# Kernel optimization log

Measured on AMD Instinct MI355X. Metric: run time of the kernel, lower is better.

The kernel has to match this reference:

```python
import jax, jax.numpy as jnp
import numpy as np

N, D_IN, D_OUT = 8192, 1024, 1024

def setup_inputs() -> dict:
    key = jax.random.key(0)
    kx, kq, kk, kv = jax.random.split(key, 4)
    s = 1.0 / np.sqrt(D_IN)
    return {
        "x": jax.random.normal(kx, (N, D_IN), dtype=jnp.float32),
        "Wq": jax.random.uniform(kq, (D_OUT, D_IN), dtype=jnp.float32, minval=-s, maxval=s),
        "Wk": jax.random.uniform(kk, (D_OUT, D_IN), dtype=jnp.float32, minval=-s, maxval=s),
        "Wv": jax.random.uniform(kv, (D_OUT, D_IN), dtype=jnp.float32, minval=-s, maxval=s),
    }

def reference(x, Wq, Wk, Wv):
    # Linear layers: y = x @ W.T (no bias, qkv_bias=False)
    q = x @ Wq.T  # [N, d_out]
    k = x @ Wk.T
    v = x @ Wv.T
    scores = q @ k.T  # [N, N]
    weights = jax.nn.softmax(scores / jnp.sqrt(jnp.float32(k.shape[-1])), axis=-1)
    return weights @ v  # [N, d_out]
```

## Files before the change

kernel.cpp:

```cpp
#include <hip/hip_runtime.h>
#include <stdint.h>

typedef __bf16 bf16_t;
typedef __bf16 bf16x8 __attribute__((ext_vector_type(8)));
typedef float f32x4 __attribute__((ext_vector_type(4)));

typedef const __attribute__((address_space(1))) void gv_t;
typedef __attribute__((address_space(3))) void lv_t;


template <int LDK>
__device__ __forceinline__ void stage_half2(const bf16_t* g, bf16_t* lh,
                                            int wave, int lane) {
#pragma unroll
  for (int i = 0; i < 2; ++i) {
    const int ub = i * 8192 + wave * 1024;
    const int o = ub + lane * 16;
    const int row = o >> 7;
    const int kb = (o & 127) ^ ((row & 7) << 4);
    const char* src = (const char*)g + (size_t)row * (LDK * 2) + kb;
    __builtin_amdgcn_global_load_lds((gv_t*)src, (lv_t*)(lh + (ub >> 1)), 16, 0, 0);
  }
}

__device__ __forceinline__ bf16x8 ld_frag2(const bf16_t* h, int r, int s, int lane) {
  int byte = r * 128 + s * 64 + ((lane >> 4) << 4);
  byte ^= (r & 7) << 4;
  return *(const bf16x8*)((const char*)h + byte);
}

template <int EPI, int MM, int NN, int KEXT, int LDK, int NKS>
__global__ __launch_bounds__(512) void gemm8p(
    const bf16_t* __restrict__ A, const bf16_t* __restrict__ Bt,
    bf16_t* __restrict__ Cb, float* __restrict__ Cf0, bf16_t* __restrict__ Cf1b,
    const float* __restrict__ rvec, float* __restrict__ partial,
    bf16_t* __restrict__ qo, bf16_t* __restrict__ ko, bf16_t* __restrict__ vtb) {
  __shared__ __align__(16) bf16_t L[2][4][8192];

  const int tid = threadIdx.x;
  const int wave = tid >> 6;
  const int lane = tid & 63;

  const int bid = blockIdx.x;
  const int x = bid & 7;
  const int j = bid >> 3;
  int tm, tn, ks;
  if (NKS > 1) {
    ks = j >> 4;
    tm = (x << 2) | (j & 3);
    tn = (j >> 2) & 3;
  } else {
    ks = 0;
    tm = (x << 2) | (j & 3);
    tn = j >> 2;
  }

  const bf16_t* Ab = A + (size_t)tm * (256 * LDK) + (size_t)ks * KEXT;
  const bf16_t* Bb = Bt + (size_t)tn * (256 * LDK) + (size_t)ks * KEXT;

  const int wr64 = (wave >> 2) * 64;
  const int wc32 = (wave & 3) * 32;
  const int fr = lane & 15;
  constexpr int nt = KEXT >> 6;

  f32x4 acc00[4][2], acc01[4][2], acc10[4][2], acc11[4][2];
#pragma unroll
  for (int m = 0; m < 4; ++m)
#pragma unroll
    for (int n = 0; n < 2; ++n) {
      acc00[m][n] = (f32x4){0.f, 0.f, 0.f, 0.f};
      acc01[m][n] = (f32x4){0.f, 0.f, 0.f, 0.f};
      acc10[m][n] = (f32x4){0.f, 0.f, 0.f, 0.f};
      acc11[m][n] = (f32x4){0.f, 0.f, 0.f, 0.f};
    }

  stage_half2<LDK>(Ab, &L[0][0][0], wave, lane);
  stage_half2<LDK>(Ab + (size_t)128 * LDK, &L[0][1][0], wave, lane);
  stage_half2<LDK>(Bb, &L[0][2][0], wave, lane);
  stage_half2<LDK>(Bb + (size_t)128 * LDK, &L[0][3][0], wave, lane);
  stage_half2<LDK>(Ab + 64, &L[1][0][0], wave, lane);
  stage_half2<LDK>(Bb + (size_t)128 * LDK + 64, &L[1][3][0], wave, lane);
  asm volatile("s_waitcnt vmcnt(4)" ::: "memory");
  __builtin_amdgcn_s_barrier();

  bf16x8 a[4][2], bA[2][2], bB[2][2];

#pragma unroll 1
  for (int t = 0; t < nt; ++t) {
    const int cur = t & 1;
    const bf16_t* A0h = &L[cur][0][0];
    const bf16_t* A1h = &L[cur][1][0];
    const bf16_t* B0h = &L[cur][2][0];
    const bf16_t* B1h = &L[cur][3][0];

#pragma unroll
    for (int m = 0; m < 4; ++m)
#pragma unroll
      for (int s = 0; s < 2; ++s)
        a[m][s] = ld_frag2(A0h, wr64 + m * 16 + fr, s, lane);
#pragma unroll
    for (int n = 0; n < 2; ++n)
#pragma unroll
      for (int s = 0; s < 2; ++s)
        bA[n][s] = ld_frag2(B0h, wc32 + n * 16 + fr, s, lane);
    if (t + 1 < nt)
      stage_half2<LDK>(Ab + (size_t)128 * LDK + (t + 1) * 64, &L[cur ^ 1][1][0],
                       wave, lane);
    __builtin_amdgcn_s_barrier();
    __builtin_amdgcn_s_setprio(1);
#pragma unroll
    for (int s = 0; s < 2; ++s)
#pragma unroll
      for (int m = 0; m < 4; ++m)
#pragma unroll
        for (int n = 0; n < 2; ++n)
          acc00[m][n] = __builtin_amdgcn_mfma_f32_16x16x32_bf16(a[m][s], bA[n][s],
                                                                acc00[m][n], 0, 0, 0);
    __builtin_amdgcn_s_setprio(0);
    __builtin_amdgcn_s_barrier();

#pragma unroll
    for (int n = 0; n < 2; ++n)
#pragma unroll
      for (int s = 0; s < 2; ++s)
        bB[n][s] = ld_frag2(B1h, wc32 + n * 16 + fr, s, lane);
    if (t + 1 < nt)
      stage_half2<LDK>(Bb + (t + 1) * 64, &L[cur ^ 1][2][0], wave, lane);
    __builtin_amdgcn_s_barrier();
    __builtin_amdgcn_s_setprio(1);
#pragma unroll
    for (int s = 0; s < 2; ++s)
#pragma unroll
      for (int m = 0; m < 4; ++m)
#pragma unroll
        for (int n = 0; n < 2; ++n)
          acc01[m][n] = __builtin_amdgcn_mfma_f32_16x16x32_bf16(a[m][s], bB[n][s],
                                                                acc01[m][n], 0, 0, 0);
    __builtin_amdgcn_s_setprio(0);
    __builtin_amdgcn_s_barrier();

#pragma unroll
    for (int m = 0; m < 4; ++m)
#pragma unroll
      for (int s = 0; s < 2; ++s)
        a[m][s] = ld_frag2(A1h, wr64 + m * 16 + fr, s, lane);
    if (t + 2 < nt)
      stage_half2<LDK>(Ab + (t + 2) * 64, &L[cur][0][0], wave, lane);
    __builtin_amdgcn_s_barrier();
    __builtin_amdgcn_s_setprio(1);
#pragma unroll
    for (int s = 0; s < 2; ++s)
#pragma unroll
      for (int m = 0; m < 4; ++m)
#pragma unroll
        for (int n = 0; n < 2; ++n)
          acc11[m][n] = __builtin_amdgcn_mfma_f32_16x16x32_bf16(a[m][s], bB[n][s],
                                                                acc11[m][n], 0, 0, 0);
    __builtin_amdgcn_s_setprio(0);
    __builtin_amdgcn_s_barrier();

    if (t + 2 < nt)
      stage_half2<LDK>(Bb + (size_t)128 * LDK + (t + 2) * 64, &L[cur][3][0],
                       wave, lane);
    __builtin_amdgcn_s_barrier();
    __builtin_amdgcn_s_setprio(1);
#pragma unroll
    for (int s = 0; s < 2; ++s)
#pragma unroll
      for (int m = 0; m < 4; ++m)
#pragma unroll
        for (int n = 0; n < 2; ++n)
          acc10[m][n] = __builtin_amdgcn_mfma_f32_16x16x32_bf16(a[m][s], bA[n][s],
                                                                acc10[m][n], 0, 0, 0);
    __builtin_amdgcn_s_setprio(0);
    if (t + 2 < nt)
      asm volatile("s_waitcnt vmcnt(4)" ::: "memory");
    else
      asm volatile("s_waitcnt vmcnt(0)" ::: "memory");
    __builtin_amdgcn_s_barrier();
  }

  const int fro = (lane >> 4) * 4;

  if (EPI == 3) {
#define EXPSTORE(ACC, QM, QN)                                                    \
  _Pragma("unroll") for (int m = 0; m < 4; ++m)                                  \
  _Pragma("unroll") for (int n = 0; n < 2; ++n)                                  \
  _Pragma("unroll") for (int jj = 0; jj < 4; ++jj) {                             \
    float e = __expf(ACC[m][n][jj]);                                             \
    ACC[m][n][jj] = e;                                                           \
    const int row = tm * 256 + QM * 128 + wr64 + m * 16 + fro + jj;              \
    const int col = tn * 256 + QN * 128 + wc32 + n * 16 + fr;                    \
    Cb[(size_t)row * NN + col] = (bf16_t)e;                                      \
  }
    EXPSTORE(acc00, 0, 0)
    EXPSTORE(acc01, 0, 1)
    EXPSTORE(acc10, 1, 0)
    EXPSTORE(acc11, 1, 1)
#undef EXPSTORE
    float* lsum = (float*)&L[0][0][0];
#define ROWSUM(A0, A1, QM)                                                       \
  _Pragma("unroll") for (int m = 0; m < 4; ++m) {                                \
    _Pragma("unroll") for (int jj = 0; jj < 4; ++jj) {                           \
      float s = A0[m][0][jj] + A0[m][1][jj] + A1[m][0][jj] + A1[m][1][jj];       \
      s += __shfl_xor(s, 1, 64);                                                 \
      s += __shfl_xor(s, 2, 64);                                                 \
      s += __shfl_xor(s, 4, 64);                                                 \
      s += __shfl_xor(s, 8, 64);                                                 \
      if (fr == 0) {                                                             \
        const int rl = QM * 128 + wr64 + m * 16 + fro + jj;                      \
        lsum[rl * 4 + (wave & 3)] = s;                                           \
      }                                                                          \
    }                                                                            \
  }
    ROWSUM(acc00, acc01, 0)
    ROWSUM(acc10, acc11, 1)
#undef ROWSUM
    __syncthreads();
    if (tid < 256) {
      float s = lsum[tid * 4] + lsum[tid * 4 + 1] + lsum[tid * 4 + 2] +
                lsum[tid * 4 + 3];
      partial[(size_t)tn * 8192 + tm * 256 + tid] = s;
    }
  } else if (EPI == 0) {
#define PVSTORE(ACC, QM, QN)                                                     \
  _Pragma("unroll") for (int m = 0; m < 4; ++m) {                                \
    const int row = tm * 256 + QM * 128 + wr64 + m * 16 + fro;                   \
    const float4 rv = *(const float4*)&rvec[row];                                \
    _Pragma("unroll") for (int n = 0; n < 2; ++n) {                              \
      const int col = tn * 256 + QN * 128 + wc32 + n * 16 + fr;                  \
      if (ks == 0) {                                                             \
        _Pragma("unroll") for (int jj = 0; jj < 4; ++jj)                         \
            Cf0[(size_t)(row + jj) * NN + col] =                                 \
                ACC[m][n][jj] * ((const float*)&rv)[jj];                         \
      } else {                                                                   \
        _Pragma("unroll") for (int jj = 0; jj < 4; ++jj)                         \
            Cf1b[(size_t)(row + jj) * NN + col] =                                \
                (bf16_t)(ACC[m][n][jj] * ((const float*)&rv)[jj]);               \
      }                                                                          \
    }                                                                            \
  }
    PVSTORE(acc00, 0, 0)
    PVSTORE(acc01, 0, 1)
    PVSTORE(acc10, 1, 0)
    PVSTORE(acc11, 1, 1)
#undef PVSTORE
  } else {
#define QKVSTORE(ACC, QM, QN)                                                    \
  _Pragma("unroll") for (int m = 0; m < 4; ++m) {                                \
    _Pragma("unroll") for (int n = 0; n < 2; ++n) {                              \
      const int row = tm * 256 + QM * 128 + wr64 + m * 16 + fro;                 \
      const int col = tn * 256 + QN * 128 + wc32 + n * 16 + fr;                  \
      if (col < 1024) {                                                          \
        _Pragma("unroll") for (int jj = 0; jj < 4; ++jj)                         \
            qo[(size_t)(row + jj) * 1024 + col] = (bf16_t)ACC[m][n][jj];         \
      } else if (col < 2048) {                                                   \
        _Pragma("unroll") for (int jj = 0; jj < 4; ++jj)                         \
            ko[(size_t)(row + jj) * 1024 + (col - 1024)] = (bf16_t)ACC[m][n][jj];\
      } else {                                                                   \
        union { bf16_t h[4]; uint2 u; } tpk;                                     \
        _Pragma("unroll") for (int jj = 0; jj < 4; ++jj)                         \
            tpk.h[jj] = (bf16_t)ACC[m][n][jj];                                   \
        *(uint2*)&vtb[(size_t)(col - 2048) * MM + row] = tpk.u;                  \
      }                                                                          \
    }                                                                            \
  }
    QKVSTORE(acc00, 0, 0)
    QKVSTORE(acc01, 0, 1)
    QKVSTORE(acc10, 1, 0)
    QKVSTORE(acc11, 1, 1)
#undef QKVSTORE
  }
}

__global__ __launch_bounds__(256) void cvt_f32_bf16(const float* __restrict__ s,
                                                    bf16_t* __restrict__ d,
                                                    int n8, float scale) {
  int i = blockIdx.x * 256 + threadIdx.x;
  if (i >= n8) return;
  const float4* sp = (const float4*)s + (size_t)i * 2;
  float4 x0 = sp[0], x1 = sp[1];
  bf16x8 o;
  o[0] = (bf16_t)(x0.x * scale);
  o[1] = (bf16_t)(x0.y * scale);
  o[2] = (bf16_t)(x0.z * scale);
  o[3] = (bf16_t)(x0.w * scale);
  o[4] = (bf16_t)(x1.x * scale);
  o[5] = (bf16_t)(x1.y * scale);
  o[6] = (bf16_t)(x1.z * scale);
  o[7] = (bf16_t)(x1.w * scale);
  ((bf16x8*)d)[i] = o;
}

__global__ __launch_bounds__(256) void rowsum_recip(const float* __restrict__ partial,
                                                    float* __restrict__ r) {
  int row = blockIdx.x * 256 + threadIdx.x;
  float s = 0.f;
#pragma unroll
  for (int t = 0; t < 32; ++t) s += partial[(size_t)t * 8192 + row];
  r[row] = 1.0f / s;
}

__global__ __launch_bounds__(256) void add_p1(float* __restrict__ out,
                                              const bf16_t* __restrict__ p1b) {
  size_t i = (size_t)blockIdx.x * 256 + threadIdx.x;
  bf16x8 b = ((const bf16x8*)p1b)[i];
  float4 a0 = ((const float4*)out)[i * 2];
  float4 a1 = ((const float4*)out)[i * 2 + 1];
  a0.x += (float)b[0];
  a0.y += (float)b[1];
  a0.z += (float)b[2];
  a0.w += (float)b[3];
  a1.x += (float)b[4];
  a1.y += (float)b[5];
  a1.z += (float)b[6];
  a1.w += (float)b[7];
  ((float4*)out)[i * 2] = a0;
  ((float4*)out)[i * 2 + 1] = a1;
}

extern "C" void kernel_launch(void* const* d_in, const int* in_sizes, int n_in,
                              void* d_out, int out_size, void* d_ws, size_t ws_size,
                              hipStream_t stream) {
  const int N = 8192, D = 1024;
  const float* x = (const float*)d_in[0];
  const float* Wq = (const float*)d_in[1];
  const float* Wk = (const float*)d_in[2];
  const float* Wv = (const float*)d_in[3];
  float* out = (float*)d_out;

  bf16_t* qb = (bf16_t*)d_ws;
  bf16_t* kb = qb + (size_t)N * D;
  bf16_t* vt = kb + (size_t)N * D;
  bf16_t* S = vt + (size_t)N * D;
  bf16_t* xb = S;
  bf16_t* Wb = xb + (size_t)N * D;
  bf16_t* P1b = qb;
  float* rvec = (float*)kb;
  float* partial = out;

  cvt_f32_bf16<<<(N * D / 8) / 256, 256, 0, stream>>>(x, xb, N * D / 8, 1.0f);
  cvt_f32_bf16<<<(D * D / 8) / 256, 256, 0, stream>>>(Wq, Wb, D * D / 8, 0.03125f);
  cvt_f32_bf16<<<(D * D / 8) / 256, 256, 0, stream>>>(Wk, Wb + (size_t)D * D,
                                                      D * D / 8, 1.0f);
  cvt_f32_bf16<<<(D * D / 8) / 256, 256, 0, stream>>>(Wv, Wb + (size_t)2 * D * D,
                                                      D * D / 8, 1.0f);

  gemm8p<2, 8192, 3072, 1024, 1024, 1><<<(N / 256) * (3 * D / 256), 512, 0, stream>>>(
      xb, Wb, nullptr, nullptr, nullptr, nullptr, nullptr, qb, kb, vt);

  gemm8p<3, 8192, 8192, 1024, 1024, 1><<<(N / 256) * (N / 256), 512, 0, stream>>>(
      qb, kb, S, nullptr, nullptr, nullptr, partial, nullptr, nullptr, nullptr);

  rowsum_recip<<<N / 256, 256, 0, stream>>>(partial, rvec);

  gemm8p<0, 8192, 1024, 4096, 8192, 2><<<(N / 256) * (D / 256) * 2, 512, 0, stream>>>(
      S, vt, nullptr, out, P1b, rvec, nullptr, nullptr, nullptr, nullptr);

  add_p1<<<(N * D / 8) / 256, 256, 0, stream>>>(out, P1b);
}
```

Baseline: 369.7 us.

## Compute QK^T scores with FP8 MFMA via dedicated scores kernel

The QKV projection now writes Q and K as FP8 (e4m3) instead of bf16, with the softmax scale split evenly across Wq and Wk as 1/sqrt(32) each. A new 128x128-tile kernel built on the MX-scaled 16x16x128 FP8 MFMA computes the scores, then applies exp, stores bf16 probabilities and writes per-row partial sums. The rowsum kernel now reduces 64 partials instead of 32. The aim is to double matrix throughput and halve operand traffic for the largest GEMM, at the cost of lower precision in the scores and smaller tiles.

Result: faster. 330.4 us (-10.6%).

```diff
diff --git a/kernel.cpp b/kernel.cpp
--- a/kernel.cpp
+++ b/kernel.cpp
@@ -4,6 +4,8 @@
 typedef __bf16 bf16_t;
 typedef __bf16 bf16x8 __attribute__((ext_vector_type(8)));
 typedef float f32x4 __attribute__((ext_vector_type(4)));
+typedef int i32x4 __attribute__((ext_vector_type(4)));
+typedef int i32x8 __attribute__((ext_vector_type(8)));
 
 typedef const __attribute__((address_space(1))) void gv_t;
 typedef __attribute__((address_space(3))) void lv_t;
@@ -32,9 +34,10 @@
 template <int EPI, int MM, int NN, int KEXT, int LDK, int NKS>
 __global__ __launch_bounds__(512) void gemm8p(
     const bf16_t* __restrict__ A, const bf16_t* __restrict__ Bt,
-    bf16_t* __restrict__ Cb, float* __restrict__ Cf0, bf16_t* __restrict__ Cf1b,
-    const float* __restrict__ rvec, float* __restrict__ partial,
-    bf16_t* __restrict__ qo, bf16_t* __restrict__ ko, bf16_t* __restrict__ vtb) {
+    float* __restrict__ Cf0, bf16_t* __restrict__ Cf1b,
+    const float* __restrict__ rvec,
+    uint8_t* __restrict__ qo, uint8_t* __restrict__ ko,
+    bf16_t* __restrict__ vtb) {
   __shared__ __align__(16) bf16_t L[2][4][8192];
 
   const int tid = threadIdx.x;
@@ -181,96 +184,156 @@
   }
 
   const int fro = (lane >> 4) * 4;
-
-  if (EPI == 3) {
-#define EXPSTORE(ACC, QM, QN)                                                    \
-  _Pragma("unroll") for (int m = 0; m < 4; ++m)                                  \
-  _Pragma("unroll") for (int n = 0; n < 2; ++n)                                  \
-  _Pragma("unroll") for (int jj = 0; jj < 4; ++jj) {                             \
-    float e = __expf(ACC[m][n][jj]);                                             \
-    ACC[m][n][jj] = e;                                                           \
-    const int row = tm * 256 + QM * 128 + wr64 + m * 16 + fro + jj;              \
-    const int col = tn * 256 + QN * 128 + wc32 + n * 16 + fr;                    \
-    Cb[(size_t)row * NN + col] = (bf16_t)e;                                      \
-  }
-    EXPSTORE(acc00, 0, 0)
-    EXPSTORE(acc01, 0, 1)
-    EXPSTORE(acc10, 1, 0)
-    EXPSTORE(acc11, 1, 1)
-#undef EXPSTORE
-    float* lsum = (float*)&L[0][0][0];
-#define ROWSUM(A0, A1, QM)                                                       \
-  _Pragma("unroll") for (int m = 0; m < 4; ++m) {                                \
-    _Pragma("unroll") for (int jj = 0; jj < 4; ++jj) {                           \
-      float s = A0[m][0][jj] + A0[m][1][jj] + A1[m][0][jj] + A1[m][1][jj];       \
-      s += __shfl_xor(s, 1, 64);                                                 \
-      s += __shfl_xor(s, 2, 64);                                                 \
-      s += __shfl_xor(s, 4, 64);                                                 \
-      s += __shfl_xor(s, 8, 64);                                                 \
-      if (fr == 0) {                                                             \
-        const int rl = QM * 128 + wr64 + m * 16 + fro + jj;                      \
-        lsum[rl * 4 + (wave & 3)] = s;                                           \
-      }                                                                          \
-    }                                                                            \
-  }
-    ROWSUM(acc00, acc01, 0)
-    ROWSUM(acc10, acc11, 1)
-#undef ROWSUM
-    __syncthreads();
-    if (tid < 256) {
-      float s = lsum[tid * 4] + lsum[tid * 4 + 1] + lsum[tid * 4 + 2] +
-                lsum[tid * 4 + 3];
-      partial[(size_t)tn * 8192 + tm * 256 + tid] = s;
-    }
-  } else if (EPI == 0) {
-#define PVSTORE(ACC, QM, QN)                                                     \
-  _Pragma("unroll") for (int m = 0; m < 4; ++m) {                                \
-    const int row = tm * 256 + QM * 128 + wr64 + m * 16 + fro;                   \
-    const float4 rv = *(const float4*)&rvec[row];                                \
-    _Pragma("unroll") for (int n = 0; n < 2; ++n) {                              \
-      const int col = tn * 256 + QN * 128 + wc32 + n * 16 + fr;                  \
-      if (ks == 0) {                                                             \
-        _Pragma("unroll") for (int jj = 0; jj < 4; ++jj)                         \
-            Cf0[(size_t)(row + jj) * NN + col] =                                 \
-                ACC[m][n][jj] * ((const float*)&rv)[jj];                         \
-      } else {                                                                   \
-        _Pragma("unroll") for (int jj = 0; jj < 4; ++jj)                         \
-            Cf1b[(size_t)(row + jj) * NN + col] =                                \
-                (bf16_t)(ACC[m][n][jj] * ((const float*)&rv)[jj]);               \
-      }                                                                          \
-    }                                                                            \
-  }
-    PVSTORE(acc00, 0, 0)
-    PVSTORE(acc01, 0, 1)
-    PVSTORE(acc10, 1, 0)
-    PVSTORE(acc11, 1, 1)
-#undef PVSTORE
-  } else {
-#define QKVSTORE(ACC, QM, QN)                                                    \
+#define STORE_QUAD(ACC, QM, QN)                                                  \
   _Pragma("unroll") for (int m = 0; m < 4; ++m) {                                \
     _Pragma("unroll") for (int n = 0; n < 2; ++n) {                              \
       const int row = tm * 256 + QM * 128 + wr64 + m * 16 + fro;                 \
       const int col = tn * 256 + QN * 128 + wc32 + n * 16 + fr;                  \
-      if (col < 1024) {                                                          \
-        _Pragma("unroll") for (int jj = 0; jj < 4; ++jj)                         \
-            qo[(size_t)(row + jj) * 1024 + col] = (bf16_t)ACC[m][n][jj];         \
-      } else if (col < 2048) {                                                   \
-        _Pragma("unroll") for (int jj = 0; jj < 4; ++jj)                         \
-            ko[(size_t)(row + jj) * 1024 + (col - 1024)] = (bf16_t)ACC[m][n][jj];\
+      if (EPI == 0) {                                                            \
+        const float4 rv = *(const float4*)&rvec[row];                            \
+        if (ks == 0) {                                                           \
+          _Pragma("unroll") for (int jj = 0; jj < 4; ++jj)                       \
+              Cf0[(size_t)(row + jj) * NN + col] =                               \
+                  ACC[m][n][jj] * ((const float*)&rv)[jj];                       \
+        } else {                                                                 \
+          _Pragma("unroll") for (int jj = 0; jj < 4; ++jj)                       \
+              Cf1b[(size_t)(row + jj) * NN + col] =                              \
+                  (bf16_t)(ACC[m][n][jj] * ((const float*)&rv)[jj]);             \
+        }                                                                        \
       } else {                                                                   \
-        union { bf16_t h[4]; uint2 u; } tpk;                                     \
-        _Pragma("unroll") for (int jj = 0; jj < 4; ++jj)                         \
-            tpk.h[jj] = (bf16_t)ACC[m][n][jj];                                   \
-        *(uint2*)&vtb[(size_t)(col - 2048) * MM + row] = tpk.u;                  \
+        if (col < 1024) {                                                        \
+          _Pragma("unroll") for (int jj = 0; jj < 4; ++jj) {                     \
+            int pk = __builtin_amdgcn_cvt_pk_fp8_f32(ACC[m][n][jj],              \
+                                                     ACC[m][n][jj], 0, false);   \
+            qo[(size_t)(row + jj) * 1024 + col] = (uint8_t)pk;                   \
+          }                                                                      \
+        } else if (col < 2048) {                                                 \
+          _Pragma("unroll") for (int jj = 0; jj < 4; ++jj) {                     \
+            int pk = __builtin_amdgcn_cvt_pk_fp8_f32(ACC[m][n][jj],              \
+                                                     ACC[m][n][jj], 0, false);   \
+            ko[(size_t)(row + jj) * 1024 + (col - 1024)] = (uint8_t)pk;          \
+          }                                                                      \
+        } else {                                                                 \
+          union { bf16_t h[4]; uint2 u; } tpk;                                   \
+          _Pragma("unroll") for (int jj = 0; jj < 4; ++jj)                       \
+              tpk.h[jj] = (bf16_t)ACC[m][n][jj];                                 \
+          *(uint2*)&vtb[(size_t)(col - 2048) * MM + row] = tpk.u;                \
+        }                                                                        \
       }                                                                          \
     }                                                                            \
   }
-    QKVSTORE(acc00, 0, 0)
-    QKVSTORE(acc01, 0, 1)
-    QKVSTORE(acc10, 1, 0)
-    QKVSTORE(acc11, 1, 1)
-#undef QKVSTORE
-  }
+  STORE_QUAD(acc00, 0, 0)
+  STORE_QUAD(acc01, 0, 1)
+  STORE_QUAD(acc10, 1, 0)
+  STORE_QUAD(acc11, 1, 1)
+#undef STORE_QUAD
+}
+
+
+__device__ __forceinline__ void stage_fp8(const uint8_t* g, uint8_t* l,
+                                          int wave, int lane) {
+#pragma unroll
+  for (int i = 0; i < 4; ++i) {
+    const int ub = i * 4096 + wave * 1024;
+    const int o = ub + lane * 16;
+    const int row = o >> 7;
+    const int col = (o & 127) ^ ((row & 7) << 4);
+    __builtin_amdgcn_global_load_lds((gv_t*)(g + (size_t)row * 1024 + col),
+                                     (lv_t*)(l + ub), 16, 0, 0);
+  }
+}
+
+__device__ __forceinline__ i32x8 ld_frag8(const uint8_t* base128, int row, int kg) {
+  const int sw = (row & 7) << 4;
+  const uint8_t* b = base128 + row * 128;
+  i32x4 lo = *(const i32x4*)(b + (kg ^ sw));
+  i32x4 hi = *(const i32x4*)(b + ((kg | 16) ^ sw));
+  i32x8 v;
+  v[0] = lo[0]; v[1] = lo[1]; v[2] = lo[2]; v[3] = lo[3];
+  v[4] = hi[0]; v[5] = hi[1]; v[6] = hi[2]; v[7] = hi[3];
+  return v;
+}
+
+__global__ __launch_bounds__(256) void scores_fp8(
+    const uint8_t* __restrict__ qf, const uint8_t* __restrict__ kf,
+    bf16_t* __restrict__ S, float* __restrict__ partial) {
+  __shared__ __align__(16) uint8_t lA[2][128 * 128];
+  __shared__ __align__(16) uint8_t lB[2][128 * 128];
+
+  const int tid = threadIdx.x;
+  const int wave = tid >> 6;
+  const int lane = tid & 63;
+
+  const int bid = blockIdx.x;
+  const int x = bid & 7;
+  const int j = bid >> 3;
+  const int tm = (x << 3) | (j & 7);
+  const int tn = j >> 3;
+
+  const uint8_t* Ab = qf + (size_t)tm * 128 * 1024;
+  const uint8_t* Bb = kf + (size_t)tn * 128 * 1024;
+
+  const int wr = (wave >> 1) * 64;
+  const int wc = (wave & 1) * 64;
+  const int fr = lane & 15;
+  const int kg = (lane >> 4) * 32;
+
+  f32x4 acc[4][4];
+#pragma unroll
+  for (int m = 0; m < 4; ++m)
+#pragma unroll
+    for (int n = 0; n < 4; ++n) acc[m][n] = (f32x4){0.f, 0.f, 0.f, 0.f};
+
+  stage_fp8(Ab, lA[0], wave, lane);
+  stage_fp8(Bb, lB[0], wave, lane);
+  __syncthreads();
+
+#pragma unroll 1
+  for (int kt = 0; kt < 8; ++kt) {
+    const int cur = kt & 1;
+    if (kt < 7) {
+      stage_fp8(Ab + (kt + 1) * 128, lA[cur ^ 1], wave, lane);
+      stage_fp8(Bb + (kt + 1) * 128, lB[cur ^ 1], wave, lane);
+    }
+    i32x8 a[4], b[4];
+#pragma unroll
+    for (int m = 0; m < 4; ++m) a[m] = ld_frag8(lA[cur], wr + m * 16 + fr, kg);
+#pragma unroll
+    for (int n = 0; n < 4; ++n) b[n] = ld_frag8(lB[cur], wc + n * 16 + fr, kg);
+#pragma unroll
+    for (int m = 0; m < 4; ++m)
+#pragma unroll
+      for (int n = 0; n < 4; ++n)
+        acc[m][n] = __builtin_amdgcn_mfma_scale_f32_16x16x128_f8f6f4(
+            a[m], b[n], acc[m][n], 0, 0, 0, 0x7F7F7F7F, 0, 0x7F7F7F7F);
+    __syncthreads();
+  }
+
+  const int fro = (lane >> 4) * 4;
+  float* lsum = (float*)&lA[0][0];
+#pragma unroll
+  for (int m = 0; m < 4; ++m) {
+#pragma unroll
+    for (int jj = 0; jj < 4; ++jj) {
+      const int rl = wr + m * 16 + fro + jj;
+      float s = 0.f;
+#pragma unroll
+      for (int n = 0; n < 4; ++n) {
+        float e = __expf(acc[m][n][jj]);
+        const int col = tn * 128 + wc + n * 16 + fr;
+        S[(size_t)(tm * 128 + rl) * 8192 + col] = (bf16_t)e;
+        s += e;
+      }
+      s += __shfl_xor(s, 1, 64);
+      s += __shfl_xor(s, 2, 64);
+      s += __shfl_xor(s, 4, 64);
+      s += __shfl_xor(s, 8, 64);
+      if (fr == 0) lsum[rl * 2 + (wave & 1)] = s;
+    }
+  }
+  __syncthreads();
+  if (tid < 128)
+    partial[(size_t)tn * 8192 + tm * 128 + tid] = lsum[tid * 2] + lsum[tid * 2 + 1];
 }
 
 __global__ __launch_bounds__(256) void cvt_f32_bf16(const float* __restrict__ s,
@@ -297,7 +360,7 @@
   int row = blockIdx.x * 256 + threadIdx.x;
   float s = 0.f;
 #pragma unroll
-  for (int t = 0; t < 32; ++t) s += partial[(size_t)t * 8192 + row];
+  for (int t = 0; t < 64; ++t) s += partial[(size_t)t * 8192 + row];
   r[row] = 1.0f / s;
 }
 
@@ -329,33 +392,34 @@
   const float* Wv = (const float*)d_in[3];
   float* out = (float*)d_out;
 
-  bf16_t* qb = (bf16_t*)d_ws;
-  bf16_t* kb = qb + (size_t)N * D;
-  bf16_t* vt = kb + (size_t)N * D;
+  uint8_t* qf = (uint8_t*)d_ws;
+  uint8_t* kf = qf + (size_t)N * D;
+  bf16_t* vt = (bf16_t*)(kf + (size_t)N * D);
   bf16_t* S = vt + (size_t)N * D;
   bf16_t* xb = S;
   bf16_t* Wb = xb + (size_t)N * D;
-  bf16_t* P1b = qb;
-  float* rvec = (float*)kb;
+  bf16_t* P1b = (bf16_t*)d_ws;
+  float* rvec = (float*)(S + (size_t)N * N);
   float* partial = out;
 
+  const float sq = 0.1767766953f;
+
   cvt_f32_bf16<<<(N * D / 8) / 256, 256, 0, stream>>>(x, xb, N * D / 8, 1.0f);
-  cvt_f32_bf16<<<(D * D / 8) / 256, 256, 0, stream>>>(Wq, Wb, D * D / 8, 0.03125f);
+  cvt_f32_bf16<<<(D * D / 8) / 256, 256, 0, stream>>>(Wq, Wb, D * D / 8, sq);
   cvt_f32_bf16<<<(D * D / 8) / 256, 256, 0, stream>>>(Wk, Wb + (size_t)D * D,
-                                                      D * D / 8, 1.0f);
+                                                      D * D / 8, sq);
   cvt_f32_bf16<<<(D * D / 8) / 256, 256, 0, stream>>>(Wv, Wb + (size_t)2 * D * D,
                                                       D * D / 8, 1.0f);
 
   gemm8p<2, 8192, 3072, 1024, 1024, 1><<<(N / 256) * (3 * D / 256), 512, 0, stream>>>(
-      xb, Wb, nullptr, nullptr, nullptr, nullptr, nullptr, qb, kb, vt);
-
-  gemm8p<3, 8192, 8192, 1024, 1024, 1><<<(N / 256) * (N / 256), 512, 0, stream>>>(
-      qb, kb, S, nullptr, nullptr, nullptr, partial, nullptr, nullptr, nullptr);
+      xb, Wb, nullptr, nullptr, nullptr, qf, kf, vt);
+
+  scores_fp8<<<(N / 128) * (N / 128), 256, 0, stream>>>(qf, kf, S, partial);
 
   rowsum_recip<<<N / 256, 256, 0, stream>>>(partial, rvec);
 
   gemm8p<0, 8192, 1024, 4096, 8192, 2><<<(N / 256) * (D / 256) * 2, 512, 0, stream>>>(
-      S, vt, nullptr, out, P1b, rvec, nullptr, nullptr, nullptr, nullptr);
+      S, vt, out, P1b, rvec, nullptr, nullptr, nullptr);
 
   add_p1<<<(N * D / 8) / 256, 256, 0, stream>>>(out, P1b);
 }
```
